# Optimization experiments

Measured on AMD Instinct MI355X. Metric: run time of the kernel, lower is better.

## Reference

```python
import jax, jax.numpy as jnp
import numpy as np

N = 50000      # nodes
E = 400000     # edges (before self loops)
IN = 128       # in_feat
HID = 64       # n_hidden per head
HEADS = [4, 4, 1]
NEG_SLOPE = 0.2  # DGL GATConv default


def gat_layer(h, src, dst, W, al, ar, b, n_nodes):
    # h: [N, Din]; W: [Din, H*F]; al/ar: [H, F]; b: [H*F]
    H, F = al.shape
    feat = (h @ W).reshape(n_nodes, H, F)              # [N,H,F]
    el = jnp.sum(feat * al, axis=-1)                   # [N,H]
    er = jnp.sum(feat * ar, axis=-1)                   # [N,H]
    e = jax.nn.leaky_relu(el[src] + er[dst], NEG_SLOPE)  # [E,H]
    # edge softmax over destination node segments (stable)
    e_max = jax.lax.stop_gradient(jax.ops.segment_max(e, dst, num_segments=n_nodes))
    ex = jnp.exp(e - e_max[dst])                       # [E,H]
    denom = jax.ops.segment_sum(ex, dst, num_segments=n_nodes)  # [N,H]
    alpha = ex / denom[dst]                            # [E,H]
    msg = feat[src] * alpha[:, :, None]                # [E,H,F]
    out = jax.ops.segment_sum(msg, dst, num_segments=n_nodes)   # [N,H,F]
    out = out + b.reshape(1, H, F)
    return out.reshape(n_nodes, H * F)


def setup_inputs() -> dict:
    key = jax.random.key(0)
    ks = jax.random.split(key, 16)
    inp = {
        "node_feat": jax.random.normal(ks[0], (N, IN), jnp.float32),
        "src": jax.random.randint(ks[1], (E,), 0, N),
        "dst": jax.random.randint(ks[2], (E,), 0, N),
    }
    dins = [IN, HID * HEADS[0], HID * HEADS[1]]
    for i, (din, h) in enumerate(zip(dins, HEADS)):
        k = 3 + 3 * i
        inp[f"W{i}"] = jax.random.normal(ks[k], (din, h * HID), jnp.float32) * 0.1
        inp[f"al{i}"] = jax.random.normal(ks[k + 1], (h, HID), jnp.float32) * 0.1
        inp[f"ar{i}"] = jax.random.normal(ks[k + 2], (h, HID), jnp.float32) * 0.1
        inp[f"b{i}"] = jnp.zeros((h * HID,), jnp.float32)
    return inp


def reference(node_feat, src, dst, W0, al0, ar0, b0, W1, al1, ar1, b1, W2, al2, ar2, b2):
    n_nodes = node_feat.shape[0]
    # add_self_loop
    loop = jnp.arange(n_nodes, dtype=src.dtype)
    src_a = jnp.concatenate([src, loop])
    dst_a = jnp.concatenate([dst, loop])
    h = node_feat
    h = gat_layer(h, src_a, dst_a, W0, al0, ar0, b0, n_nodes)  # [N, 4*64]
    h = gat_layer(h, src_a, dst_a, W1, al1, ar1, b1, n_nodes)  # [N, 4*64]
    h = gat_layer(h, src_a, dst_a, W2, al2, ar2, b2, n_nodes)  # [N, 64]
    return h
```

## Files before the change

kernel.cpp:

```cpp
#include <hip/hip_runtime.h>


typedef __attribute__((ext_vector_type(8))) short short8;
typedef __attribute__((ext_vector_type(4))) float f32x4;
typedef __attribute__((ext_vector_type(2))) float f32x2;
typedef __attribute__((ext_vector_type(4))) int int4v;

__device__ __forceinline__ float bf2f(ushort u) {
  union { unsigned int i; float f; } c;
  c.i = ((unsigned int)u) << 16;
  return c.f;
}
__device__ __forceinline__ ushort f2bf(float f) {
  union { float f; unsigned int i; } c;
  c.f = f;
  unsigned int u = c.i;
  u += 0x7FFFu + ((u >> 16) & 1u);
  return (ushort)(u >> 16);
}
__device__ __forceinline__ f32x2 bfp2(uint u) {
  union { unsigned int i; float f; } lo, hi;
  lo.i = u << 16;
  hi.i = u & 0xFFFF0000u;
  f32x2 r;
  r[0] = lo.f;
  r[1] = hi.f;
  return r;
}
__device__ __forceinline__ float lrelu_exp(float x) {
  const float y = fmaxf(x, 0.2f * x);
  return __expf(y);
}
__device__ __forceinline__ void gload_lds16(const ushort* g, void* lds) {
  __builtin_amdgcn_global_load_lds(
      (const __attribute__((address_space(1))) unsigned int*)g,
      (__attribute__((address_space(3))) unsigned int*)lds, 16, 0, 0);
}

__global__ __launch_bounds__(256) void prep_kernel(
    const float* __restrict__ nf, ushort* __restrict__ a0, int n8, int nbA,
    const float* __restrict__ W0, ushort* __restrict__ Wt0,
    const float* __restrict__ W1, ushort* __restrict__ Wt1,
    const float* __restrict__ W2, ushort* __restrict__ Wt2, int nbW,
    int* __restrict__ cnt, int Nn, int nbZ, int* __restrict__ esrc, int ETP,
    int nbE, ushort* __restrict__ feat_sent, float* __restrict__ el4,
    float* __restrict__ el1) {
  const int b = blockIdx.x;
  if (b < nbA) {
    const int i = b * 256 + threadIdx.x;
    if (i >= n8) return;
    const float4 v0 = ((const float4*)nf)[i * 2];
    const float4 v1 = ((const float4*)nf)[i * 2 + 1];
    short8 o;
    o[0] = (short)f2bf(v0.x); o[1] = (short)f2bf(v0.y);
    o[2] = (short)f2bf(v0.z); o[3] = (short)f2bf(v0.w);
    o[4] = (short)f2bf(v1.x); o[5] = (short)f2bf(v1.y);
    o[6] = (short)f2bf(v1.z); o[7] = (short)f2bf(v1.w);
    ((short8*)a0)[i] = o;
  } else if (b < nbA + nbW) {
    const int i = (b - nbA) * 256 + threadIdx.x;
    if (i < 32768) {
      const int k = i >> 8, n = i & 255;
      Wt0[n * 128 + k] = f2bf(W0[i]);
    } else if (i < 32768 + 65536) {
      const int j = i - 32768;
      const int k = j >> 8, n = j & 255;
      Wt1[n * 256 + k] = f2bf(W1[j]);
    } else if (i < 32768 + 65536 + 16384) {
      const int j = i - 32768 - 65536;
      const int k = j >> 6, n = j & 63;
      Wt2[n * 256 + k] = f2bf(W2[j]);
    }
  } else if (b < nbA + nbW + nbZ) {
    const int idx = (b - nbA - nbW) * 256 + threadIdx.x;
    const int base = idx * 4;
    if (base + 4 <= Nn) {
      ((int4v*)cnt)[idx] = (int4v)0;
    } else if (base < Nn) {
      for (int j = base; j < Nn; ++j) cnt[j] = 0;
    }
  } else if (b < nbA + nbW + nbZ + nbE) {
    const int idx = (b - nbA - nbW - nbZ) * 256 + threadIdx.x;
    const int base = idx * 4;
    if (base + 4 <= ETP) {
      ((int4*)esrc)[idx] = make_int4(Nn, Nn, Nn, Nn);
    } else if (base < ETP) {
      for (int j = base; j < ETP; ++j) esrc[j] = Nn;
    }
  } else {
    const int t = threadIdx.x;
    if (t < 128) ((uint*)feat_sent)[t] = 0u;
    if (t >= 128 && t < 132) el4[(size_t)Nn * 4 + (t - 128)] = -1e9f;
    if (t == 132) el1[Nn] = -1e9f;
  }
}

__global__ __launch_bounds__(256) void gemm_h4(
    const ushort* __restrict__ A, const ushort* __restrict__ Wt,
    ushort* __restrict__ C, int M, int K, const float* __restrict__ al,
    const float* __restrict__ ar, float* __restrict__ el,
    float* __restrict__ er) {
  __shared__ ushort As[64][64];
  __shared__ ushort Bs[256][64];
  const int bm = blockIdx.x * 64;
  const int tid = threadIdx.x;
  const int lane = tid & 63;
  const int wave = tid >> 6;
  const int lrow = lane >> 3;
  const int lslot = lane & 7;

  f32x4 acc[4][4];
#pragma unroll
  for (int m = 0; m < 4; ++m)
#pragma unroll
    for (int n = 0; n < 4; ++n) acc[m][n] = 0.f;

  for (int k0 = 0; k0 < K; k0 += 64) {
#pragma unroll
    for (int j = 0; j < 2; ++j) {
      const int c = wave * 2 + j;
      const int row = c * 8 + lrow;
      int rg = bm + row;
      if (rg >= M) rg = M - 1;
      const int kcol = (lslot ^ (row & 7)) * 8;
      gload_lds16(A + (size_t)rg * K + k0 + kcol,
                  (char*)(&As[0][0]) + c * 1024 + lrow * 128 + lslot * 16);
    }
#pragma unroll
    for (int j = 0; j < 8; ++j) {
      const int c = wave * 8 + j;
      const int row = c * 8 + lrow;
      const int kcol = (lslot ^ (row & 7)) * 8;
      gload_lds16(Wt + (size_t)row * K + k0 + kcol,
                  (char*)(&Bs[0][0]) + c * 1024 + lrow * 128 + lslot * 16);
    }
    __syncthreads();

#pragma unroll
    for (int kk = 0; kk < 2; ++kk) {
      short8 a[4], b[4];
#pragma unroll
      for (int m = 0; m < 4; ++m) {
        const int row = m * 16 + (lane & 15);
        const int slot = (kk * 4 + (lane >> 4)) ^ (row & 7);
        a[m] = *(const short8*)((const char*)&As[0][0] + row * 128 + slot * 16);
      }
#pragma unroll
      for (int n = 0; n < 4; ++n) {
        const int row = wave * 64 + n * 16 + (lane & 15);
        const int slot = (kk * 4 + (lane >> 4)) ^ (row & 7);
        b[n] = *(const short8*)((const char*)&Bs[0][0] + row * 128 + slot * 16);
      }
#pragma unroll
      for (int m = 0; m < 4; ++m)
#pragma unroll
        for (int n = 0; n < 4; ++n)
          acc[m][n] = __builtin_amdgcn_mfma_f32_16x16x32_bf16(
              a[m], b[n], acc[m][n], 0, 0, 0);
    }
    __syncthreads();
  }

  const int cc = lane & 15;
  float alv[4], arv[4];
#pragma unroll
  for (int n = 0; n < 4; ++n) {
    alv[n] = al[wave * 64 + n * 16 + cc];
    arv[n] = ar[wave * 64 + n * 16 + cc];
  }
#pragma unroll
  for (int m = 0; m < 4; ++m) {
#pragma unroll
    for (int r = 0; r < 4; ++r) {
      const int row = bm + m * 16 + (lane >> 4) * 4 + r;
      const bool ok = row < M;
      if (ok) {
#pragma unroll
        for (int n = 0; n < 4; ++n) {
          const int col = wave * 64 + n * 16 + cc;
          C[(size_t)row * 256 + col] = f2bf(acc[m][n][r]);
        }
      }
      float pl = 0.f, pr = 0.f;
#pragma unroll
      for (int n = 0; n < 4; ++n) {
        pl = fmaf(acc[m][n][r], alv[n], pl);
        pr = fmaf(acc[m][n][r], arv[n], pr);
      }
#pragma unroll
      for (int o = 1; o < 16; o <<= 1) {
        pl += __shfl_xor(pl, o);
        pr += __shfl_xor(pr, o);
      }
      if (cc == 0 && ok) {
        el[row * 4 + wave] = pl;
        er[row * 4 + wave] = pr;
      }
    }
  }
}

__global__ __launch_bounds__(256) void gemm_h1(
    const ushort* __restrict__ A, const ushort* __restrict__ Wt,
    ushort* __restrict__ C, int M, int K, const float* __restrict__ al,
    const float* __restrict__ ar, float* __restrict__ el,
    float* __restrict__ er) {
  constexpr int BN = 64, NF = 2, NCHB = 8;
  __shared__ ushort As[128][64];
  __shared__ ushort Bs[BN][64];
  const int bm = blockIdx.x * 128;
  const int tid = threadIdx.x;
  const int lane = tid & 63;
  const int wave = tid >> 6;
  const int wm = wave >> 1;
  const int wn = wave & 1;
  const int lrow = lane >> 3;
  const int lslot = lane & 7;

  f32x4 acc[4][NF];
#pragma unroll
  for (int m = 0; m < 4; ++m)
#pragma unroll
    for (int n = 0; n < NF; ++n) acc[m][n] = 0.f;

  for (int k0 = 0; k0 < K; k0 += 64) {
#pragma unroll
    for (int c = wave; c < 16; c += 4) {
      const int row = c * 8 + lrow;
      int rg = bm + row;
      if (rg >= M) rg = M - 1;
      const int kcol = (lslot ^ (row & 7)) * 8;
      gload_lds16(A + (size_t)rg * K + k0 + kcol,
                  (char*)(&As[0][0]) + c * 1024 + lrow * 128 + lslot * 16);
    }
#pragma unroll
    for (int c = wave; c < NCHB; c += 4) {
      const int row = c * 8 + lrow;
      const int kcol = (lslot ^ (row & 7)) * 8;
      gload_lds16(Wt + (size_t)row * K + k0 + kcol,
                  (char*)(&Bs[0][0]) + c * 1024 + lrow * 128 + lslot * 16);
    }
    __syncthreads();

#pragma unroll
    for (int kk = 0; kk < 2; ++kk) {
      short8 a[4], b[NF];
#pragma unroll
      for (int m = 0; m < 4; ++m) {
        const int row = wm * 64 + m * 16 + (lane & 15);
        const int slot = (kk * 4 + (lane >> 4)) ^ (row & 7);
        a[m] = *(const short8*)((const char*)&As[0][0] + row * 128 + slot * 16);
      }
#pragma unroll
      for (int n = 0; n < NF; ++n) {
        const int row = wn * 32 + n * 16 + (lane & 15);
        const int slot = (kk * 4 + (lane >> 4)) ^ (row & 7);
        b[n] = *(const short8*)((const char*)&Bs[0][0] + row * 128 + slot * 16);
      }
#pragma unroll
      for (int m = 0; m < 4; ++m)
#pragma unroll
        for (int n = 0; n < NF; ++n)
          acc[m][n] = __builtin_amdgcn_mfma_f32_16x16x32_bf16(
              a[m], b[n], acc[m][n], 0, 0, 0);
    }
    __syncthreads();
  }

#pragma unroll
  for (int m = 0; m < 4; ++m) {
#pragma unroll
    for (int r = 0; r < 4; ++r) {
      const int row = bm + wm * 64 + m * 16 + (lane >> 4) * 4 + r;
      if (row < M) {
#pragma unroll
        for (int n = 0; n < NF; ++n) {
          const int col = wn * 32 + n * 16 + (lane & 15);
          C[(size_t)row * 64 + col] = f2bf(acc[m][n][r]);
        }
      }
    }
  }

  float* red = (float*)&As[0][0];
  const int cc = lane & 15;
  const int q = lane >> 4;
  float alv[NF], arv[NF];
#pragma unroll
  for (int n = 0; n < NF; ++n) {
    alv[n] = al[wn * 32 + n * 16 + cc];
    arv[n] = ar[wn * 32 + n * 16 + cc];
  }
#pragma unroll
  for (int m = 0; m < 4; ++m) {
#pragma unroll
    for (int r = 0; r < 4; ++r) {
      float pl = 0.f, pr = 0.f;
#pragma unroll
      for (int n = 0; n < NF; ++n) {
        pl = fmaf(acc[m][n][r], alv[n], pl);
        pr = fmaf(acc[m][n][r], arv[n], pr);
      }
#pragma unroll
      for (int o = 1; o < 16; o <<= 1) {
        pl += __shfl_xor(pl, o);
        pr += __shfl_xor(pr, o);
      }
      if (cc == 0) {
        const int rl = wm * 64 + m * 16 + q * 4 + r;
        red[rl * 2 + wn] = pl;
        red[256 + rl * 2 + wn] = pr;
      }
    }
  }
  __syncthreads();
  if (tid < 128) {
    const int row = bm + tid;
    if (row < M) {
      el[row] = red[tid * 2] + red[tid * 2 + 1];
      er[row] = red[256 + tid * 2] + red[256 + tid * 2 + 1];
    }
  }
}

__global__ void hist_kernel(const int* __restrict__ dst, int* __restrict__ cnt,
                            int E, int Nn) {
  const int e = blockIdx.x * blockDim.x + threadIdx.x;
  if (e >= E + Nn) return;
  const int d = (e < E) ? dst[e] : (e - E);
  atomicAdd(&cnt[d], 1);
}

__device__ __forceinline__ int block_incl_scan_1024(int x, int* lds16) {
  const int lane = threadIdx.x & 63;
  const int wid = threadIdx.x >> 6;
  int inc = x;
#pragma unroll
  for (int off = 1; off < 64; off <<= 1) {
    const int y = __shfl_up(inc, off);
    if (lane >= off) inc += y;
  }
  if (lane == 63) lds16[wid] = inc;
  __syncthreads();
  if (wid == 0) {
    int t = (lane < 16) ? lds16[lane] : 0;
#pragma unroll
    for (int off = 1; off < 16; off <<= 1) {
      const int y = __shfl_up(t, off);
      if (lane >= off) t += y;
    }
    if (lane < 16) lds16[lane] = t;
  }
  __syncthreads();
  if (wid > 0) inc += lds16[wid - 1];
  return inc;
}

__global__ __launch_bounds__(1024) void scan_blocks_kernel(
    const int* __restrict__ cnt, int* __restrict__ row_ptr,
    int* __restrict__ partials, int n) {
  __shared__ int lds16[16];
  const int i = blockIdx.x * 1024 + threadIdx.x;
  const int x = (i < n) ? ((cnt[i] + 3) & ~3) : 0;
  const int inc = block_incl_scan_1024(x, lds16);
  if (i < n) row_ptr[i] = inc - x;
  if (threadIdx.x == 1023) partials[blockIdx.x] = inc;
}

__global__ __launch_bounds__(1024) void scan_partials_kernel(
    int* __restrict__ partials, int* __restrict__ row_ptr, int nb, int n) {
  __shared__ int lds16[16];
  const int x = (threadIdx.x < nb) ? partials[threadIdx.x] : 0;
  const int inc = block_incl_scan_1024(x, lds16);
  if (threadIdx.x < nb) partials[threadIdx.x] = inc - x;
  if (threadIdx.x == nb - 1) row_ptr[n] = inc;
}

__global__ __launch_bounds__(1024) void add_offsets_kernel(
    int* __restrict__ row_ptr, int* __restrict__ cursor,
    const int* __restrict__ partials, int n) {
  const int i = blockIdx.x * 1024 + threadIdx.x;
  if (i < n) {
    const int v = row_ptr[i] + partials[blockIdx.x];
    row_ptr[i] = v;
    cursor[i] = v;
  }
}

__global__ void scatter_kernel(const int* __restrict__ src,
                               const int* __restrict__ dst,
                               int* __restrict__ cursor, int* __restrict__ esrc,
                               int E, int Nn) {
  const int e = blockIdx.x * blockDim.x + threadIdx.x;
  if (e >= E + Nn) return;
  const int s = (e < E) ? src[e] : (e - E);
  const int d = (e < E) ? dst[e] : (e - E);
  const int pos = atomicAdd(&cursor[d], 1);
  esrc[pos] = s;
}

__global__ __launch_bounds__(256) void agg_fused_h4(
    const int* __restrict__ row_ptr, const int* __restrict__ esrc,
    const float* __restrict__ el, const float* __restrict__ er,
    const ushort* __restrict__ feat, const float* __restrict__ b,
    ushort* __restrict__ out, int Nn) {
  const int n = (blockIdx.x * 256 + threadIdx.x) >> 6;
  const int lane = threadIdx.x & 63;
  if (n >= Nn) return;
  const int h = lane >> 4;
  const int start = row_ptr[n];
  const int end = row_ptr[n + 1];
  const float erv = er[n * 4 + h];
  const uint2* fb = (const uint2*)feat + lane;

  float den = 0.f;
  f32x2 acc01 = 0.f, acc23 = 0.f;
  for (int i = start; i < end; i += 4) {
    const int4 s = *(const int4*)(esrc + i);
    const float x0 = el[s.x * 4 + h];
    const float x1 = el[s.y * 4 + h];
    const float x2 = el[s.z * 4 + h];
    const float x3 = el[s.w * 4 + h];
    const uint2 f0 = fb[(size_t)s.x * 64];
    const uint2 f1 = fb[(size_t)s.y * 64];
    const uint2 f2 = fb[(size_t)s.z * 64];
    const uint2 f3 = fb[(size_t)s.w * 64];
    const float e0 = lrelu_exp(x0 + erv), e1 = lrelu_exp(x1 + erv),
                e2 = lrelu_exp(x2 + erv), e3 = lrelu_exp(x3 + erv);
    den += (e0 + e1) + (e2 + e3);
    acc01 += bfp2(f0.x) * e0;
    acc23 += bfp2(f0.y) * e0;
    acc01 += bfp2(f1.x) * e1;
    acc23 += bfp2(f1.y) * e1;
    acc01 += bfp2(f2.x) * e2;
    acc23 += bfp2(f2.y) * e2;
    acc01 += bfp2(f3.x) * e3;
    acc23 += bfp2(f3.y) * e3;
  }
  const float rden = 1.f / den;
  const float4 bb = ((const float4*)b)[lane];
  short4 o;
  o.x = (short)f2bf(acc01[0] * rden + bb.x);
  o.y = (short)f2bf(acc01[1] * rden + bb.y);
  o.z = (short)f2bf(acc23[0] * rden + bb.z);
  o.w = (short)f2bf(acc23[1] * rden + bb.w);
  ((short4*)out)[(size_t)n * 64 + lane] = o;
}

__global__ __launch_bounds__(256) void agg_fused_h1(
    const int* __restrict__ row_ptr, const int* __restrict__ esrc,
    const float* __restrict__ el, const float* __restrict__ er,
    const ushort* __restrict__ feat, const float* __restrict__ b,
    float* __restrict__ out, int Nn) {
  const int wid = (blockIdx.x * 256 + threadIdx.x) >> 6;
  const int lane = threadIdx.x & 63;
  const int n = wid * 2 + (lane >> 5);
  const int sub = lane & 31;
  if (n >= Nn) return;
  const int start = row_ptr[n];
  const int end = row_ptr[n + 1];
  const float erv = er[n];
  const uint* fb = (const uint*)feat + sub;

  float den = 0.f;
  f32x2 acc = 0.f;
  for (int i = start; i < end; i += 4) {
    const int4 s = *(const int4*)(esrc + i);
    const float x0 = el[s.x], x1 = el[s.y], x2 = el[s.z], x3 = el[s.w];
    const uint f0 = fb[(size_t)s.x * 32];
    const uint f1 = fb[(size_t)s.y * 32];
    const uint f2 = fb[(size_t)s.z * 32];
    const uint f3 = fb[(size_t)s.w * 32];
    const float e0 = lrelu_exp(x0 + erv), e1 = lrelu_exp(x1 + erv),
                e2 = lrelu_exp(x2 + erv), e3 = lrelu_exp(x3 + erv);
    den += (e0 + e1) + (e2 + e3);
    acc += bfp2(f0) * e0;
    acc += bfp2(f1) * e1;
    acc += bfp2(f2) * e2;
    acc += bfp2(f3) * e3;
  }
  const float rden = 1.f / den;
  const float2 bb = ((const float2*)b)[sub];
  float2 o;
  o.x = acc[0] * rden + bb.x;
  o.y = acc[1] * rden + bb.y;
  ((float2*)out)[(size_t)n * 32 + sub] = o;
}

extern "C" void kernel_launch(void* const* d_in, const int* in_sizes, int n_in,
                              void* d_out, int out_size, void* d_ws,
                              size_t ws_size, hipStream_t stream) {
  const float* nf = (const float*)d_in[0];
  const int* src = (const int*)d_in[1];
  const int* dst = (const int*)d_in[2];
  const float* W0 = (const float*)d_in[3];
  const float* al0 = (const float*)d_in[4];
  const float* ar0 = (const float*)d_in[5];
  const float* b0 = (const float*)d_in[6];
  const float* W1 = (const float*)d_in[7];
  const float* al1 = (const float*)d_in[8];
  const float* ar1 = (const float*)d_in[9];
  const float* b1 = (const float*)d_in[10];
  const float* W2 = (const float*)d_in[11];
  const float* al2 = (const float*)d_in[12];
  const float* ar2 = (const float*)d_in[13];
  const float* b2 = (const float*)d_in[14];

  const int IN = 128;
  const int Nn = in_sizes[0] / IN;
  const int E = in_sizes[1];
  const int ETP = E + 4 * Nn;

  char* ws = (char*)d_ws;
  size_t off = 0;
  auto alloc = [&](size_t bytes) {
    char* p = ws + off;
    off += (bytes + 255) & ~(size_t)255;
    return p;
  };
  ushort* feat = (ushort*)alloc(((size_t)Nn + 1) * 256 * 2);
  ushort* h1 = (ushort*)alloc((size_t)Nn * 256 * 2);
  ushort* h2 = (ushort*)alloc((size_t)Nn * 256 * 2);
  ushort* a0 = (ushort*)alloc((size_t)Nn * 128 * 2);
  ushort* Wt0 = (ushort*)alloc((size_t)256 * 128 * 2);
  ushort* Wt1 = (ushort*)alloc((size_t)256 * 256 * 2);
  ushort* Wt2 = (ushort*)alloc((size_t)64 * 256 * 2);
  float* el4 = (float*)alloc(((size_t)Nn + 1) * 4 * 4);
  float* er4 = (float*)alloc((size_t)Nn * 4 * 4);
  float* el1 = (float*)alloc(((size_t)Nn + 1) * 4);
  float* er1 = (float*)alloc((size_t)Nn * 4);
  int* row_ptr = (int*)alloc(((size_t)Nn + 1) * 4);
  int* cnt = (int*)alloc((size_t)Nn * 4);
  int* cursor = (int*)alloc((size_t)Nn * 4);
  int* esrc = (int*)alloc((size_t)ETP * 4);
  int* partials = (int*)alloc((size_t)1024 * 4);
  (void)ws_size;
  (void)n_in;
  (void)out_size;

  const int n8 = Nn * 16;
  const int nbA = (n8 + 255) / 256;
  const int nbW = (32768 + 65536 + 16384 + 255) / 256;
  const int nbZ = (Nn + 1023) / 1024;
  const int nbE = (ETP + 1023) / 1024;
  prep_kernel<<<nbA + nbW + nbZ + nbE + 1, 256, 0, stream>>>(
      nf, a0, n8, nbA, W0, Wt0, W1, Wt1, W2, Wt2, nbW, cnt, Nn, nbZ, esrc,
      ETP, nbE, feat + (size_t)Nn * 256, el4, el1);

  const int ET = E + Nn;
  const int nb = (Nn + 1023) / 1024;
  hist_kernel<<<(ET + 255) / 256, 256, 0, stream>>>(dst, cnt, E, Nn);
  scan_blocks_kernel<<<nb, 1024, 0, stream>>>(cnt, row_ptr, partials, Nn);
  scan_partials_kernel<<<1, 1024, 0, stream>>>(partials, row_ptr, nb, Nn);
  add_offsets_kernel<<<nb, 1024, 0, stream>>>(row_ptr, cursor, partials, Nn);
  scatter_kernel<<<(ET + 255) / 256, 256, 0, stream>>>(src, dst, cursor, esrc,
                                                       E, Nn);

  const int waves_grid = (Nn * 64 + 255) / 256;
  const int gemm_grid = (Nn + 63) / 64;

  gemm_h4<<<gemm_grid, 256, 0, stream>>>(a0, Wt0, feat, Nn, 128, al0, ar0,
                                         el4, er4);
  agg_fused_h4<<<waves_grid, 256, 0, stream>>>(row_ptr, esrc, el4, er4, feat,
                                               b0, h1, Nn);
  gemm_h4<<<gemm_grid, 256, 0, stream>>>(h1, Wt1, feat, Nn, 256, al1, ar1,
                                         el4, er4);
  agg_fused_h4<<<waves_grid, 256, 0, stream>>>(row_ptr, esrc, el4, er4, feat,
                                               b1, h2, Nn);
  gemm_h1<<<(Nn + 127) / 128, 256, 0, stream>>>(h2, Wt2, feat, Nn, 256, al2,
                                                ar2, el1, er1);
  agg_fused_h1<<<(Nn * 32 + 255) / 256, 256, 0, stream>>>(
      row_ptr, esrc, el1, er1, feat, b2, (float*)d_out, Nn);
}
```

Baseline: 209.4 us.

## Fuse prep and CSR construction into one cooperative kernel with grid syncs

```diff
diff --git a/kernel.cpp b/kernel.cpp
--- a/kernel.cpp
+++ b/kernel.cpp
@@ -1,10 +1,12 @@
 #include <hip/hip_runtime.h>
+#include <hip/hip_cooperative_groups.h>
+
+namespace cg = cooperative_groups;
 
 
 typedef __attribute__((ext_vector_type(8))) short short8;
 typedef __attribute__((ext_vector_type(4))) float f32x4;
 typedef __attribute__((ext_vector_type(2))) float f32x2;
-typedef __attribute__((ext_vector_type(4))) int int4v;
 
 __device__ __forceinline__ float bf2f(ushort u) {
   union { unsigned int i; float f; } c;
@@ -37,18 +39,47 @@
       (__attribute__((address_space(3))) unsigned int*)lds, 16, 0, 0);
 }
 
-__global__ __launch_bounds__(256) void prep_kernel(
-    const float* __restrict__ nf, ushort* __restrict__ a0, int n8, int nbA,
+__device__ __forceinline__ int block_incl_scan_1024(int x, int* lds16) {
+  const int lane = threadIdx.x & 63;
+  const int wid = threadIdx.x >> 6;
+  int inc = x;
+#pragma unroll
+  for (int off = 1; off < 64; off <<= 1) {
+    const int y = __shfl_up(inc, off);
+    if (lane >= off) inc += y;
+  }
+  if (lane == 63) lds16[wid] = inc;
+  __syncthreads();
+  if (wid == 0) {
+    int t = (lane < 16) ? lds16[lane] : 0;
+#pragma unroll
+    for (int off = 1; off < 16; off <<= 1) {
+      const int y = __shfl_up(t, off);
+      if (lane >= off) t += y;
+    }
+    if (lane < 16) lds16[lane] = t;
+  }
+  __syncthreads();
+  if (wid > 0) inc += lds16[wid - 1];
+  return inc;
+}
+
+__global__ __launch_bounds__(1024) void csr_coop(
+    const float* __restrict__ nf, ushort* __restrict__ a0, int n8,
     const float* __restrict__ W0, ushort* __restrict__ Wt0,
     const float* __restrict__ W1, ushort* __restrict__ Wt1,
-    const float* __restrict__ W2, ushort* __restrict__ Wt2, int nbW,
-    int* __restrict__ cnt, int Nn, int nbZ, int* __restrict__ esrc, int ETP,
-    int nbE, ushort* __restrict__ feat_sent, float* __restrict__ el4,
-    float* __restrict__ el1) {
-  const int b = blockIdx.x;
-  if (b < nbA) {
-    const int i = b * 256 + threadIdx.x;
-    if (i >= n8) return;
+    const float* __restrict__ W2, ushort* __restrict__ Wt2,
+    const int* __restrict__ src, const int* __restrict__ dst,
+    int* __restrict__ cnt, int* __restrict__ row_ptr, int* __restrict__ cursor,
+    int* __restrict__ esrc, int* __restrict__ partials,
+    float* __restrict__ el4, float* __restrict__ el1,
+    ushort* __restrict__ feat_sent, int E, int Nn, int ETP) {
+  cg::grid_group grid = cg::this_grid();
+  __shared__ int lds16[16];
+  const int gtid = blockIdx.x * 1024 + threadIdx.x;
+  const int gsz = gridDim.x * 1024;
+
+  for (int i = gtid; i < n8; i += gsz) {
     const float4 v0 = ((const float4*)nf)[i * 2];
     const float4 v1 = ((const float4*)nf)[i * 2 + 1];
     short8 o;
@@ -57,8 +88,8 @@
     o[4] = (short)f2bf(v1.x); o[5] = (short)f2bf(v1.y);
     o[6] = (short)f2bf(v1.z); o[7] = (short)f2bf(v1.w);
     ((short8*)a0)[i] = o;
-  } else if (b < nbA + nbW) {
-    const int i = (b - nbA) * 256 + threadIdx.x;
+  }
+  for (int i = gtid; i < 32768 + 65536 + 16384; i += gsz) {
     if (i < 32768) {
       const int k = i >> 8, n = i & 255;
       Wt0[n * 128 + k] = f2bf(W0[i]);
@@ -66,32 +97,52 @@
       const int j = i - 32768;
       const int k = j >> 8, n = j & 255;
       Wt1[n * 256 + k] = f2bf(W1[j]);
-    } else if (i < 32768 + 65536 + 16384) {
+    } else {
       const int j = i - 32768 - 65536;
       const int k = j >> 6, n = j & 63;
       Wt2[n * 256 + k] = f2bf(W2[j]);
     }
-  } else if (b < nbA + nbW + nbZ) {
-    const int idx = (b - nbA - nbW) * 256 + threadIdx.x;
-    const int base = idx * 4;
-    if (base + 4 <= Nn) {
-      ((int4v*)cnt)[idx] = (int4v)0;
-    } else if (base < Nn) {
-      for (int j = base; j < Nn; ++j) cnt[j] = 0;
-    }
-  } else if (b < nbA + nbW + nbZ + nbE) {
-    const int idx = (b - nbA - nbW - nbZ) * 256 + threadIdx.x;
-    const int base = idx * 4;
-    if (base + 4 <= ETP) {
-      ((int4*)esrc)[idx] = make_int4(Nn, Nn, Nn, Nn);
-    } else if (base < ETP) {
-      for (int j = base; j < ETP; ++j) esrc[j] = Nn;
-    }
-  } else {
-    const int t = threadIdx.x;
-    if (t < 128) ((uint*)feat_sent)[t] = 0u;
-    if (t >= 128 && t < 132) el4[(size_t)Nn * 4 + (t - 128)] = -1e9f;
-    if (t == 132) el1[Nn] = -1e9f;
+  }
+  for (int i = gtid; i < Nn; i += gsz) cnt[i] = 0;
+  for (int i = gtid; i < ETP; i += gsz) esrc[i] = Nn;
+  if (gtid < 4) el4[(size_t)Nn * 4 + gtid] = -1e9f;
+  if (gtid == 4) el1[Nn] = -1e9f;
+  if (gtid >= 64 && gtid < 192) ((uint*)feat_sent)[gtid - 64] = 0u;
+  grid.sync();
+
+  const int ET = E + Nn;
+  for (int e = gtid; e < ET; e += gsz) {
+    const int d = (e < E) ? dst[e] : (e - E);
+    atomicAdd(&cnt[d], 1);
+  }
+  grid.sync();
+
+  const int x = (gtid < Nn) ? ((cnt[gtid] + 3) & ~3) : 0;
+  const int inc = block_incl_scan_1024(x, lds16);
+  if (gtid < Nn) row_ptr[gtid] = inc - x;
+  if (threadIdx.x == 1023) partials[blockIdx.x] = inc;
+  grid.sync();
+
+  if (blockIdx.x == 0) {
+    const int nbk = gridDim.x;
+    const int xx = (threadIdx.x < nbk) ? partials[threadIdx.x] : 0;
+    const int inc2 = block_incl_scan_1024(xx, lds16);
+    if (threadIdx.x < nbk) partials[threadIdx.x] = inc2 - xx;
+    if (threadIdx.x == nbk - 1) row_ptr[Nn] = inc2;
+  }
+  grid.sync();
+
+  if (gtid < Nn) {
+    const int v = row_ptr[gtid] + partials[blockIdx.x];
+    row_ptr[gtid] = v;
+    cursor[gtid] = v;
+  }
+  grid.sync();
+
+  for (int e = gtid; e < ET; e += gsz) {
+    const int s = (e < E) ? src[e] : (e - E);
+    const int d = (e < E) ? dst[e] : (e - E);
+    esrc[atomicAdd(&cursor[d], 1)] = s;
   }
 }
 
@@ -205,9 +256,9 @@
     ushort* __restrict__ C, int M, int K, const float* __restrict__ al,
     const float* __restrict__ ar, float* __restrict__ el,
     float* __restrict__ er) {
-  constexpr int BN = 64, NF = 2, NCHB = 8;
+  constexpr int NF = 2, NCHB = 8;
   __shared__ ushort As[128][64];
-  __shared__ ushort Bs[BN][64];
+  __shared__ ushort Bs[64][64];
   const int bm = blockIdx.x * 128;
   const int tid = threadIdx.x;
   const int lane = tid & 63;
@@ -321,82 +372,6 @@
       er[row] = red[256 + tid * 2] + red[256 + tid * 2 + 1];
     }
   }
-}
-
-__global__ void hist_kernel(const int* __restrict__ dst, int* __restrict__ cnt,
-                            int E, int Nn) {
-  const int e = blockIdx.x * blockDim.x + threadIdx.x;
-  if (e >= E + Nn) return;
-  const int d = (e < E) ? dst[e] : (e - E);
-  atomicAdd(&cnt[d], 1);
-}
-
-__device__ __forceinline__ int block_incl_scan_1024(int x, int* lds16) {
-  const int lane = threadIdx.x & 63;
-  const int wid = threadIdx.x >> 6;
-  int inc = x;
-#pragma unroll
-  for (int off = 1; off < 64; off <<= 1) {
-    const int y = __shfl_up(inc, off);
-    if (lane >= off) inc += y;
-  }
-  if (lane == 63) lds16[wid] = inc;
-  __syncthreads();
-  if (wid == 0) {
-    int t = (lane < 16) ? lds16[lane] : 0;
-#pragma unroll
-    for (int off = 1; off < 16; off <<= 1) {
-      const int y = __shfl_up(t, off);
-      if (lane >= off) t += y;
-    }
-    if (lane < 16) lds16[lane] = t;
-  }
-  __syncthreads();
-  if (wid > 0) inc += lds16[wid - 1];
-  return inc;
-}
-
-__global__ __launch_bounds__(1024) void scan_blocks_kernel(
-    const int* __restrict__ cnt, int* __restrict__ row_ptr,
-    int* __restrict__ partials, int n) {
-  __shared__ int lds16[16];
-  const int i = blockIdx.x * 1024 + threadIdx.x;
-  const int x = (i < n) ? ((cnt[i] + 3) & ~3) : 0;
-  const int inc = block_incl_scan_1024(x, lds16);
-  if (i < n) row_ptr[i] = inc - x;
-  if (threadIdx.x == 1023) partials[blockIdx.x] = inc;
-}
-
-__global__ __launch_bounds__(1024) void scan_partials_kernel(
-    int* __restrict__ partials, int* __restrict__ row_ptr, int nb, int n) {
-  __shared__ int lds16[16];
-  const int x = (threadIdx.x < nb) ? partials[threadIdx.x] : 0;
-  const int inc = block_incl_scan_1024(x, lds16);
-  if (threadIdx.x < nb) partials[threadIdx.x] = inc - x;
-  if (threadIdx.x == nb - 1) row_ptr[n] = inc;
-}
-
-__global__ __launch_bounds__(1024) void add_offsets_kernel(
-    int* __restrict__ row_ptr, int* __restrict__ cursor,
-    const int* __restrict__ partials, int n) {
-  const int i = blockIdx.x * 1024 + threadIdx.x;
-  if (i < n) {
-    const int v = row_ptr[i] + partials[blockIdx.x];
-    row_ptr[i] = v;
-    cursor[i] = v;
-  }
-}
-
-__global__ void scatter_kernel(const int* __restrict__ src,
-                               const int* __restrict__ dst,
-                               int* __restrict__ cursor, int* __restrict__ esrc,
-                               int E, int Nn) {
-  const int e = blockIdx.x * blockDim.x + threadIdx.x;
-  if (e >= E + Nn) return;
-  const int s = (e < E) ? src[e] : (e - E);
-  const int d = (e < E) ? dst[e] : (e - E);
-  const int pos = atomicAdd(&cursor[d], 1);
-  esrc[pos] = s;
 }
 
 __global__ __launch_bounds__(256) void agg_fused_h4(
@@ -538,23 +513,21 @@
   (void)n_in;
   (void)out_size;
 
-  const int n8 = Nn * 16;
-  const int nbA = (n8 + 255) / 256;
-  const int nbW = (32768 + 65536 + 16384 + 255) / 256;
-  const int nbZ = (Nn + 1023) / 1024;
-  const int nbE = (ETP + 1023) / 1024;
-  prep_kernel<<<nbA + nbW + nbZ + nbE + 1, 256, 0, stream>>>(
-      nf, a0, n8, nbA, W0, Wt0, W1, Wt1, W2, Wt2, nbW, cnt, Nn, nbZ, esrc,
-      ETP, nbE, feat + (size_t)Nn * 256, el4, el1);
-
-  const int ET = E + Nn;
-  const int nb = (Nn + 1023) / 1024;
-  hist_kernel<<<(ET + 255) / 256, 256, 0, stream>>>(dst, cnt, E, Nn);
-  scan_blocks_kernel<<<nb, 1024, 0, stream>>>(cnt, row_ptr, partials, Nn);
-  scan_partials_kernel<<<1, 1024, 0, stream>>>(partials, row_ptr, nb, Nn);
-  add_offsets_kernel<<<nb, 1024, 0, stream>>>(row_ptr, cursor, partials, Nn);
-  scatter_kernel<<<(ET + 255) / 256, 256, 0, stream>>>(src, dst, cursor, esrc,
-                                                       E, Nn);
+  {
+    int n8 = Nn * 16;
+    ushort* feat_sent = feat + (size_t)Nn * 256;
+    void* args[] = {&nf, &a0, &n8, &W0, &Wt0, &W1, &Wt1, &W2, &Wt2,
+                    &src, &dst, &cnt, &row_ptr, &cursor, &esrc, &partials,
+                    &el4, &el1, &feat_sent, (void*)&E, (void*)&Nn,
+                    (void*)&ETP};
+    int EE = E, NN = Nn, ET = ETP;
+    void* args2[] = {&nf, &a0, &n8, &W0, &Wt0, &W1, &Wt1, &W2, &Wt2,
+                     &src, &dst, &cnt, &row_ptr, &cursor, &esrc, &partials,
+                     &el4, &el1, &feat_sent, &EE, &NN, &ET};
+    (void)args;
+    hipLaunchCooperativeKernel((const void*)csr_coop, dim3(128), dim3(1024),
+                               args2, 0, stream);
+  }
 
   const int waves_grid = (Nn * 64 + 255) / 256;
   const int gemm_grid = (Nn + 63) / 64;
```

Result: slower. 299.2 us (+42.9%).
